# Kernel tuning notes

Hardware: AMD Instinct MI355X
Metric: run time of the kernel (lower is better)

The kernel has to match this reference:

```python
import jax, jax.numpy as jnp
import numpy as np

EPS = 1e-5        # torch BatchNorm2d default eps
G = 8             # DCNv4 groups
KP = 9            # 3x3 kernel points


def conv2d(x, w):
    return jax.lax.conv_general_dilated(
        x, w, window_strides=(1, 1), padding='SAME',
        dimension_numbers=('NCHW', 'OIHW', 'NCHW'))


def bn_eval(x, g_, b_, m_, v_):
    s = g_ / jnp.sqrt(v_ + EPS)
    return x * s[None, :, None, None] + (b_ - m_ * s)[None, :, None, None]


def silu(x):
    return x * jax.nn.sigmoid(x)


def dcnv4_core(value, offset, mask):
    # value: (N,H,W,G,Cg)  offset: (N,H,W,G,K,2) (x,y)  mask: (N,H,W,G,K) unnormalized (DCNv4: no softmax)
    N, H, W, Gn, Cg = value.shape
    r = jnp.arange(-1, 2, dtype=value.dtype)              # dilation=1, pad=1, 3x3 grid
    gy, gx = jnp.meshgrid(r, r, indexing='ij')
    grid_x = gx.ravel()  # (9,)
    grid_y = gy.ravel()
    px = jnp.arange(W, dtype=value.dtype)[None, None, :, None, None] + grid_x + offset[..., 0]
    py = jnp.arange(H, dtype=value.dtype)[None, :, None, None, None] + grid_y + offset[..., 1]
    x0 = jnp.floor(px); y0 = jnp.floor(py)
    lx = px - x0; ly = py - y0
    x0i = x0.astype(jnp.int32); y0i = y0.astype(jnp.int32)
    bidx = jnp.arange(N)[:, None, None, None, None]
    gidx = jnp.arange(Gn)[None, None, None, :, None]

    def tap(yi, xi, wgt):
        valid = (yi >= 0) & (yi < H) & (xi >= 0) & (xi < W)   # zero padding outside
        v = value[bidx, jnp.clip(yi, 0, H - 1), jnp.clip(xi, 0, W - 1), gidx]  # (N,H,W,G,K,Cg)
        return v * (wgt * valid)[..., None]

    s = (tap(y0i, x0i, (1 - ly) * (1 - lx))
         + tap(y0i, x0i + 1, (1 - ly) * lx)
         + tap(y0i + 1, x0i, ly * (1 - lx))
         + tap(y0i + 1, x0i + 1, ly * lx))
    return jnp.einsum('nhwgkc,nhwgk->nhwgc', s, mask)


def dcnv4(x, val_w, val_b, om_w, om_b, outp_w, outp_b):
    # x: NCHW. DCNv4 wrapper: flatten to tokens, value_proj, offset_mask linear on raw tokens,
    # deformable aggregation, output_proj, back to NCHW.
    N, C, H, W = x.shape
    t = x.transpose(0, 2, 3, 1).reshape(N, H * W, C)
    value = (t @ val_w.T + val_b).reshape(N, H, W, G, C // G)
    om = (t @ om_w.T + om_b).reshape(N, H, W, G, KP * 3)  # per group: 2K offsets then K masks
    offset = om[..., :2 * KP].reshape(N, H, W, G, KP, 2)
    mask = om[..., 2 * KP:]
    out = dcnv4_core(value, offset, mask).reshape(N, H * W, C)
    out = out @ outp_w.T + outp_b
    return out.reshape(N, H, W, C).transpose(0, 3, 1, 2)


def setup_inputs() -> dict:
    key = jax.random.key(0)
    ks = jax.random.split(key, 32)
    W_SC = 0.05
    d = {}
    d['x'] = jax.random.normal(ks[0], (4, 256, 64, 64), jnp.float32)
    d['cv1_w'] = jax.random.normal(ks[1], (128, 256, 3, 3), jnp.float32) * W_SC
    d['cv1_bn_g'] = jax.random.uniform(ks[2], (128,), jnp.float32, 0.5, 1.5)
    d['cv1_bn_b'] = jax.random.normal(ks[3], (128,), jnp.float32) * 0.1
    d['cv1_bn_m'] = jax.random.normal(ks[4], (128,), jnp.float32) * 0.1
    d['cv1_bn_v'] = jax.random.uniform(ks[5], (128,), jnp.float32, 0.5, 1.5)
    d['cv2_w'] = jax.random.normal(ks[6], (256, 128, 3, 3), jnp.float32) * W_SC
    d['cv2_bn_g'] = jax.random.uniform(ks[7], (256,), jnp.float32, 0.5, 1.5)
    d['cv2_bn_b'] = jax.random.normal(ks[8], (256,), jnp.float32) * 0.1
    d['cv2_bn_m'] = jax.random.normal(ks[9], (256,), jnp.float32) * 0.1
    d['cv2_bn_v'] = jax.random.uniform(ks[10], (256,), jnp.float32, 0.5, 1.5)
    d['val_w'] = jax.random.normal(ks[11], (256, 256), jnp.float32) * W_SC
    d['val_b'] = jax.random.normal(ks[12], (256,), jnp.float32) * 0.01
    d['om_w'] = jax.random.normal(ks[13], (216, 256), jnp.float32) * 0.02
    d['om_b'] = jax.random.normal(ks[14], (216,), jnp.float32) * 0.01
    d['outp_w'] = jax.random.normal(ks[15], (256, 256), jnp.float32) * W_SC
    d['outp_b'] = jax.random.normal(ks[16], (256,), jnp.float32) * 0.01
    d['bn3_g'] = jax.random.uniform(ks[17], (256,), jnp.float32, 0.5, 1.5)
    d['bn3_b'] = jax.random.normal(ks[18], (256,), jnp.float32) * 0.1
    d['bn3_m'] = jax.random.normal(ks[19], (256,), jnp.float32) * 0.1
    d['bn3_v'] = jax.random.uniform(ks[20], (256,), jnp.float32, 0.5, 1.5)
    d['pw1_w'] = jax.random.normal(ks[21], (768, 256, 1, 1), jnp.float32) * W_SC
    d['pw1_b'] = jax.random.normal(ks[22], (768,), jnp.float32) * 0.01
    d['pw2_w'] = jax.random.normal(ks[23], (256, 768, 1, 1), jnp.float32) * W_SC
    d['pw2_b'] = jax.random.normal(ks[24], (256,), jnp.float32) * 0.01
    return d


def reference(x, cv1_w, cv1_bn_g, cv1_bn_b, cv1_bn_m, cv1_bn_v,
              cv2_w, cv2_bn_g, cv2_bn_b, cv2_bn_m, cv2_bn_v,
              val_w, val_b, om_w, om_b, outp_w, outp_b,
              bn3_g, bn3_b, bn3_m, bn3_v, pw1_w, pw1_b, pw2_w, pw2_b):
    # cv2(cv1(x)) branch: Conv = Conv2d(no bias) + BN + SiLU
    y = silu(bn_eval(conv2d(x, cv1_w), cv1_bn_g, cv1_bn_b, cv1_bn_m, cv1_bn_v))
    y = silu(bn_eval(conv2d(y, cv2_w), cv2_bn_g, cv2_bn_b, cv2_bn_m, cv2_bn_v))
    # dcn branch: DCNv4 -> BN -> 1x1 conv (+SiLU) -> 1x1 conv
    d = dcnv4(x, val_w, val_b, om_w, om_b, outp_w, outp_b)
    d = bn_eval(d, bn3_g, bn3_b, bn3_m, bn3_v)
    d = silu(conv2d(d, pw1_w) + pw1_b[None, :, None, None])
    d = conv2d(d, pw2_w) + pw2_b[None, :, None, None]
    return x + y + d
```

## Files before the change

kernel.cpp:

```cpp
#include <hip/hip_runtime.h>
#include <math.h>

typedef __attribute__((ext_vector_type(8))) __bf16 bf16x8;
typedef __attribute__((ext_vector_type(8))) unsigned short us8;
typedef __attribute__((ext_vector_type(4))) unsigned short us4;
typedef __attribute__((ext_vector_type(4))) float f32x4;
typedef __attribute__((ext_vector_type(4))) int i32x4;
typedef unsigned int uint32;

#define EPSV 1e-5f

__device__ __forceinline__ float silu_f(float v) { return v / (1.f + __expf(-v)); }

__device__ __forceinline__ unsigned short f2bf(float f) {
  uint32 u = __builtin_bit_cast(uint32, f);
  u += 0x7fffu + ((u >> 16) & 1u);
  return (unsigned short)(u >> 16);
}
__device__ __forceinline__ float bf2f(unsigned short h) {
  uint32 u = ((uint32)h) << 16;
  return __builtin_bit_cast(float, u);
}

__device__ __forceinline__ int xswz(int b, int n) {
  return (b & 7) * (n >> 3) + (b >> 3);
}

__device__ __forceinline__ void gl_lds16(const void* g, void* l) {
  __builtin_amdgcn_global_load_lds(
      (const __attribute__((address_space(1))) unsigned int*)g,
      (__attribute__((address_space(3))) unsigned int*)l, 16, 0, 0);
}

template <int EPI, int CIN, int BN>
__device__ __forceinline__ void gemm_body(
    int rb, int cb, int k0, int KL,
    const unsigned short* __restrict__ A, const unsigned short* __restrict__ Bw,
    const float* __restrict__ bias, int K, int Co, void* __restrict__ outv,
    const float* __restrict__ e0, const float* __restrict__ e1,
    const float* __restrict__ e2, const float* __restrict__ e3,
    const unsigned short* __restrict__ zpage, bf16x8* smem) {
  constexpr int NFR = BN / 32;
  constexpr int NB = BN / 64;
  constexpr int CPB = 512 + BN * 4;
  const int t = threadIdx.x;
  const int lane = t & 63;
  const int wv = t >> 6;
  const int wr = wv >> 1, wc = wv & 1;

  f32x4 acc[4][NFR];
#pragma unroll
  for (int i = 0; i < 4; i++)
#pragma unroll
    for (int j = 0; j < NFR; j++) acc[i][j] = (f32x4){0.f, 0.f, 0.f, 0.f};

  const unsigned short* Abase[2];
  int aprow[2], apcol[2], akoff[2];
#pragma unroll
  for (int i = 0; i < 2; i++) {
    int c = t + 256 * i;
    int row = (c >> 6) * 16 + (c & 15);
    int koff = ((c >> 4) & 3) * 8;
    akoff[i] = koff;
    int grow = rb + row;
    if constexpr (CIN > 0) {
      int n = grow >> 12, p = grow & 4095;
      aprow[i] = p >> 6;
      apcol[i] = p & 63;
      Abase[i] = A + (size_t)n * 4096 * CIN;
    } else {
      Abase[i] = A + (size_t)grow * K + koff;
    }
  }
  const unsigned short* Bbase[NB];
#pragma unroll
  for (int i = 0; i < NB; i++) {
    int c = t + 256 * i;
    int col = cb + (c >> 6) * 16 + (c & 15);
    int koff = ((c >> 4) & 3) * 8;
    Bbase[i] = (col < Co) ? (Bw + (size_t)col * K + koff) : zpage;
  }
  auto addrA = [&](int i, int kb) -> const unsigned short* {
    if constexpr (CIN > 0) {
      int tap = kb / CIN;
      int ci = (kb & (CIN - 1)) + akoff[i];
      int dy = tap / 3 - 1, dx = tap % 3 - 1;
      int h = aprow[i] + dy, w = apcol[i] + dx;
      if (((unsigned)h < 64u) & ((unsigned)w < 64u))
        return &Abase[i][(size_t)(h * 64 + w) * CIN + ci];
      return zpage;
    } else {
      return Abase[i] + kb;
    }
  };
  auto stage = [&](int buf, int kb) {
    bf16x8* base = &smem[buf * CPB];
    gl_lds16(addrA(0, kb), (void*)&base[t]);
    gl_lds16(addrA(1, kb), (void*)&base[t + 256]);
    gl_lds16((Bbase[0] == zpage) ? zpage : Bbase[0] + kb, (void*)&base[512 + t]);
    if constexpr (NB == 2)
      gl_lds16((Bbase[1] == zpage) ? zpage : Bbase[1] + kb,
               (void*)&base[512 + t + 256]);
  };

  const int nt = KL >> 5;
  stage(0, k0);
  __syncthreads();
  int cur = 0;
  for (int it = 0; it < nt; ++it) {
    if (it + 1 < nt) stage(cur ^ 1, k0 + ((it + 1) << 5));
    const bf16x8* Ab = &smem[cur * CPB];
    const bf16x8* Bb = Ab + 512;
    bf16x8 af[4], bfr[NFR];
#pragma unroll
    for (int mi = 0; mi < 4; mi++) af[mi] = Ab[(wr * 4 + mi) * 64 + lane];
#pragma unroll
    for (int ni = 0; ni < NFR; ni++) bfr[ni] = Bb[(wc * NFR + ni) * 64 + lane];
    __builtin_amdgcn_s_setprio(1);
#pragma unroll
    for (int mi = 0; mi < 4; mi++)
#pragma unroll
      for (int ni = 0; ni < NFR; ni++)
        acc[mi][ni] = __builtin_amdgcn_mfma_f32_16x16x32_bf16(af[mi], bfr[ni],
                                                              acc[mi][ni], 0, 0, 0);
    __builtin_amdgcn_s_setprio(0);
    __syncthreads();
    cur ^= 1;
  }

  const int lr = lane & 15, kg4 = (lane >> 4) * 4;
#pragma unroll
  for (int mi = 0; mi < 4; mi++) {
#pragma unroll
    for (int ni = 0; ni < NFR; ni++) {
      int gcol = cb + wc * (BN / 2) + ni * 16 + lr;
      if (gcol >= Co) continue;
      float bval, s = 1.f, tt = 0.f;
      if (EPI == 2 || EPI == 7) bval = 0.f;
      else if (EPI == 5) bval = (gcol < 256) ? bias[gcol] : e0[gcol - 256];
      else bval = bias[gcol];
      if (EPI == 2 || EPI == 3) {
        s = e0[gcol] * rsqrtf(e3[gcol] + EPSV);
        tt = e1[gcol] - e2[gcol] * s;
      }
      if (EPI == 6) {
        int grow0 = rb + wr * 64 + mi * 16 + kg4;
        int n = grow0 >> 12, p0 = grow0 & 4095;
        size_t oix = ((size_t)(n * 256 + gcol)) * 4096 + p0;
        f32x4 xv = *(const f32x4*)&((const float*)e0)[oix];
        const unsigned short* y2p = (const unsigned short*)e1;
        f32x4 ov;
#pragma unroll
        for (int j = 0; j < 4; j++) {
          float y2 = bf2f(y2p[((size_t)(n * 4096 + p0 + j)) * 256 + gcol]);
          ov[j] = acc[mi][ni][j] + bval + xv[j] + y2;
        }
        *(f32x4*)&((float*)outv)[oix] = ov;
        continue;
      }
#pragma unroll
      for (int j = 0; j < 4; j++) {
        int grow = rb + wr * 64 + mi * 16 + kg4 + j;
        float v = acc[mi][ni][j] + bval;
        if (EPI == 2) v = silu_f(v * s + tt);
        if (EPI == 3) v = v * s + tt;
        if (EPI == 4) v = silu_f(v);
        if (EPI == 5) {
          if (gcol < 256)
            ((unsigned short*)outv)[(size_t)grow * 256 + gcol] = f2bf(v);
          else
            ((float*)e1)[(size_t)grow * 216 + (gcol - 256)] = v;
        } else {
          ((unsigned short*)outv)[(size_t)grow * Co + gcol] = f2bf(v);
        }
      }
    }
  }
}

__device__ __forceinline__ void dcn_body(
    int bid, const unsigned short* __restrict__ value,
    const float* __restrict__ om, unsigned short* __restrict__ out,
    void* smemraw) {
  f32x4* wgt = (f32x4*)smemraw;
  i32x4* adr = (i32x4*)((char*)smemraw + 288 * 16);
  const int n = bid >> 10;
  const int p0 = (bid & 1023) * 4;
  const int t = threadIdx.x;

  for (int idx = t; idx < 288; idx += 256) {
    int pi = idx / 72;
    int gk = idx - pi * 72;
    int g = gk / 9, k = gk - g * 9;
    int p = p0 + pi;
    int h0 = p >> 6, w0 = p & 63;
    const float* omp = om + ((size_t)(n * 4096 + p)) * 216 + g * 27;
    float ox = omp[2 * k], oy = omp[2 * k + 1], mk = omp[18 + k];
    float px = (float)(w0 + (k % 3) - 1) + ox;
    float py = (float)(h0 + (k / 3) - 1) + oy;
    float x0f = floorf(px), y0f = floorf(py);
    float lx = px - x0f, ly = py - y0f;
    int x0 = (int)x0f, y0 = (int)y0f;
    int x1 = x0 + 1, y1 = y0 + 1;
    bool vx0 = (unsigned)x0 < 64u, vx1 = (unsigned)x1 < 64u;
    bool vy0 = (unsigned)y0 < 64u, vy1 = (unsigned)y1 < 64u;
    int cx0 = min(max(x0, 0), 63), cx1 = min(max(x1, 0), 63);
    int cy0 = min(max(y0, 0), 63), cy1 = min(max(y1, 0), 63);
    f32x4 w4;
    w4[0] = (1.f - ly) * (1.f - lx) * mk * (float)(vy0 && vx0);
    w4[1] = (1.f - ly) * lx * mk * (float)(vy0 && vx1);
    w4[2] = ly * (1.f - lx) * mk * (float)(vy1 && vx0);
    w4[3] = ly * lx * mk * (float)(vy1 && vx1);
    i32x4 a4;
    a4[0] = (cy0 * 64 + cx0) * 256;
    a4[1] = (cy0 * 64 + cx1) * 256;
    a4[2] = (cy1 * 64 + cx0) * 256;
    a4[3] = (cy1 * 64 + cx1) * 256;
    wgt[idx] = w4;
    adr[idx] = a4;
  }
  __syncthreads();

  const int pi = t >> 6;
  const int g = (t >> 3) & 7;
  const int l = t & 7;
  const int p = p0 + pi;
  const unsigned short* vb = value + ((size_t)n * 4096) * 256 + g * 32 + l * 4;
  const int bix = (pi * 8 + g) * 9;
  float a0 = 0.f, a1 = 0.f, a2 = 0.f, a3 = 0.f;
#pragma unroll
  for (int k = 0; k < 9; k++) {
    f32x4 wv = wgt[bix + k];
    i32x4 av = adr[bix + k];
    us4 q0 = *(const us4*)(vb + av[0]);
    us4 q1 = *(const us4*)(vb + av[1]);
    us4 q2 = *(const us4*)(vb + av[2]);
    us4 q3 = *(const us4*)(vb + av[3]);
    a0 += wv[0] * bf2f(q0[0]) + wv[1] * bf2f(q1[0]) + wv[2] * bf2f(q2[0]) + wv[3] * bf2f(q3[0]);
    a1 += wv[0] * bf2f(q0[1]) + wv[1] * bf2f(q1[1]) + wv[2] * bf2f(q2[1]) + wv[3] * bf2f(q3[1]);
    a2 += wv[0] * bf2f(q0[2]) + wv[1] * bf2f(q1[2]) + wv[2] * bf2f(q2[2]) + wv[3] * bf2f(q3[2]);
    a3 += wv[0] * bf2f(q0[3]) + wv[1] * bf2f(q1[3]) + wv[2] * bf2f(q2[3]) + wv[3] * bf2f(q3[3]);
  }
  us4 o;
  o[0] = f2bf(a0); o[1] = f2bf(a1); o[2] = f2bf(a2); o[3] = f2bf(a3);
  *(us4*)&out[((size_t)(n * 4096 + p)) * 256 + g * 32 + l * 4] = o;
}

__global__ __launch_bounds__(256) void prep_k(
    const float* __restrict__ x, unsigned short* __restrict__ xt,
    const float* __restrict__ c1, unsigned short* __restrict__ o1,
    const float* __restrict__ c2, unsigned short* __restrict__ o2,
    const float* __restrict__ a0, unsigned short* __restrict__ b0,
    const float* __restrict__ a1, unsigned short* __restrict__ b1,
    const float* __restrict__ a2, unsigned short* __restrict__ b2,
    const float* __restrict__ a3, unsigned short* __restrict__ b3,
    const float* __restrict__ a4, unsigned short* __restrict__ b4,
    uint32* __restrict__ zp) {
  __shared__ float lds[64][65];
  int b = blockIdx.x;
  const int t = threadIdx.x;
  if (b == 0 && t < 32) zp[t] = 0u;
  if (b < 1024) {
    const int p0 = (b & 63) * 64, c0 = ((b >> 6) & 3) * 64, n = b >> 8;
    const int pp = t & 63, ccb = t >> 6;
    const float* xb = x + ((size_t)n * 256 + c0) * 4096 + p0;
#pragma unroll
    for (int i = 0; i < 16; i++) {
      int cc = ccb * 16 + i;
      lds[pp][cc] = xb[(size_t)cc * 4096 + pp];
    }
    __syncthreads();
#pragma unroll
    for (int i = 0; i < 2; i++) {
      int pp2 = (t >> 3) + i * 32;
      int c8 = (t & 7) * 8;
      us8 v;
#pragma unroll
      for (int j = 0; j < 8; j++) v[j] = f2bf(lds[pp2][c8 + j]);
      *(us8*)&xt[((size_t)(n * 4096 + p0 + pp2)) * 256 + c0 + c8] = v;
    }
    return;
  }
  if (b < 1152) {
    int idx = (b - 1024) * 256 + t;
    int co = idx >> 8, ci = idx & 255;
    const float* src = c1 + (size_t)(co * 256 + ci) * 9;
#pragma unroll
    for (int tap = 0; tap < 9; tap++)
      o1[(size_t)(co * 9 + tap) * 256 + ci] = f2bf(src[tap]);
    return;
  }
  if (b < 1280) {
    int idx = (b - 1152) * 256 + t;
    int co = idx >> 7, ci = idx & 127;
    const float* src = c2 + (size_t)(co * 128 + ci) * 9;
#pragma unroll
    for (int tap = 0; tap < 9; tap++)
      o2[(size_t)(co * 9 + tap) * 128 + ci] = f2bf(src[tap]);
    return;
  }
  int idx = (b - 1280) * 256 + t;
  const float* s;
  unsigned short* d;
  int off;
  if (idx < 65536)       { s = a0; d = b0; off = idx; }
  else if (idx < 120832) { s = a1; d = b1; off = idx - 65536; }
  else if (idx < 186368) { s = a2; d = b2; off = idx - 120832; }
  else if (idx < 382976) { s = a3; d = b3; off = idx - 186368; }
  else if (idx < 579584) { s = a4; d = b4; off = idx - 382976; }
  else return;
  d[off] = f2bf(s[off]);
}

__global__ __launch_bounds__(256) void fused_s1(
    const unsigned short* __restrict__ xt,
    const unsigned short* __restrict__ wc1, unsigned short* __restrict__ part,
    const unsigned short* __restrict__ wval, const float* __restrict__ val_b,
    const float* __restrict__ om_b, float* __restrict__ omf,
    unsigned short* __restrict__ valt, const unsigned short* __restrict__ zpage) {
  __shared__ bf16x8 smem[2048];
  int l = xswz(blockIdx.x, 1024);
  if ((l & 1) == 0) {
    int c = l >> 1;
    int s = c >> 7, mt = c & 127;
    gemm_body<7, 256, 128>(mt * 128, 0, s * 576, 576, xt, wc1, nullptr, 2304,
                           128, part + (size_t)s * 2097152, nullptr, nullptr,
                           nullptr, nullptr, zpage, smem);
  } else {
    int v = l >> 1;
    gemm_body<5, 0, 128>((v >> 2) * 128, (v & 3) * 128, 0, 256, xt, wval, val_b,
                         256, 472, valt, om_b, (const float*)omf, nullptr,
                         nullptr, zpage, smem);
  }
}

__global__ __launch_bounds__(256) void fused_r(
    const unsigned short* __restrict__ part, const float* __restrict__ g1,
    const float* __restrict__ bb1, const float* __restrict__ m1,
    const float* __restrict__ v1, unsigned short* __restrict__ y1t,
    const unsigned short* __restrict__ valt, const float* __restrict__ omf,
    unsigned short* __restrict__ dcnt) {
  __shared__ char rsm[9216];
  int l = xswz(blockIdx.x, 5120);
  int q = l / 5, r5 = l - q * 5;
  if (r5 == 0) {
    int g = q * 256 + threadIdx.x;
    int grow = g >> 4;
    int co8 = (g & 15) << 3;
    size_t base = (size_t)grow * 128 + co8;
    float sum[8] = {0.f, 0.f, 0.f, 0.f, 0.f, 0.f, 0.f, 0.f};
#pragma unroll
    for (int s = 0; s < 4; s++) {
      us8 pv = *(const us8*)&part[base + (size_t)s * 2097152];
#pragma unroll
      for (int j = 0; j < 8; j++) sum[j] += bf2f(pv[j]);
    }
    us8 o;
#pragma unroll
    for (int j = 0; j < 8; j++) {
      int co = co8 + j;
      float sc = g1[co] * rsqrtf(v1[co] + EPSV);
      float tt = bb1[co] - m1[co] * sc;
      o[j] = f2bf(silu_f(sum[j] * sc + tt));
    }
    *(us8*)&y1t[base] = o;
  } else {
    dcn_body(q * 4 + r5 - 1, valt, omf, dcnt, (void*)rsm);
  }
}

__global__ __launch_bounds__(256) void fused_s2(
    const unsigned short* __restrict__ y1t,
    const unsigned short* __restrict__ wc2, const float* __restrict__ g2,
    const float* __restrict__ bb2, const float* __restrict__ m2,
    const float* __restrict__ v2, unsigned short* __restrict__ y2t,
    const unsigned short* __restrict__ dcnt, const unsigned short* __restrict__ woutp,
    const float* __restrict__ outp_b, const float* __restrict__ g3,
    const float* __restrict__ bb3, const float* __restrict__ m3,
    const float* __restrict__ v3, unsigned short* __restrict__ d1t,
    const unsigned short* __restrict__ zpage) {
  __shared__ bf16x8 smem[1536];
  int l = xswz(blockIdx.x, 1024);
  if ((l & 1) == 0) {
    int c = l >> 1;
    gemm_body<2, 128, 64>((c >> 2) * 128, (c & 3) * 64, 0, 1152, y1t, wc2,
                          nullptr, 1152, 256, y2t, g2, bb2, m2, v2, zpage, smem);
  } else {
    int v = l >> 1;
    gemm_body<3, 0, 64>((v >> 2) * 128, (v & 3) * 64, 0, 256, dcnt, woutp,
                        outp_b, 256, 256, d1t, g3, bb3, m3, v3, zpage, smem);
  }
}

template <int EPI, int CIN, int BN, int NCB, int GRID>
__global__ __launch_bounds__(256) void gemm_k(
    const unsigned short* __restrict__ A, const unsigned short* __restrict__ Bw,
    const float* __restrict__ bias, int K, int Co, void* __restrict__ outv,
    const float* __restrict__ e0, const float* __restrict__ e1,
    const float* __restrict__ e2, const float* __restrict__ e3,
    const unsigned short* __restrict__ zpage) {
  __shared__ bf16x8 smem[2 * (512 + BN * 4)];
  int l = xswz(blockIdx.x, GRID);
  gemm_body<EPI, CIN, BN>((l / NCB) * 128, (l % NCB) * BN, 0, K, A, Bw, bias,
                          K, Co, outv, e0, e1, e2, e3, zpage, smem);
}

extern "C" void kernel_launch(void* const* d_in, const int* in_sizes, int n_in,
                              void* d_out, int out_size, void* d_ws,
                              size_t ws_size, hipStream_t stream) {
  const float* x      = (const float*)d_in[0];
  const float* cv1_w  = (const float*)d_in[1];
  const float* cv1_g  = (const float*)d_in[2];
  const float* cv1_b  = (const float*)d_in[3];
  const float* cv1_m  = (const float*)d_in[4];
  const float* cv1_v  = (const float*)d_in[5];
  const float* cv2_w  = (const float*)d_in[6];
  const float* cv2_g  = (const float*)d_in[7];
  const float* cv2_b  = (const float*)d_in[8];
  const float* cv2_m  = (const float*)d_in[9];
  const float* cv2_v  = (const float*)d_in[10];
  const float* val_w  = (const float*)d_in[11];
  const float* val_b  = (const float*)d_in[12];
  const float* om_w   = (const float*)d_in[13];
  const float* om_b   = (const float*)d_in[14];
  const float* outp_w = (const float*)d_in[15];
  const float* outp_b = (const float*)d_in[16];
  const float* bn3_g  = (const float*)d_in[17];
  const float* bn3_b  = (const float*)d_in[18];
  const float* bn3_m  = (const float*)d_in[19];
  const float* bn3_v  = (const float*)d_in[20];
  const float* pw1_w  = (const float*)d_in[21];
  const float* pw1_b  = (const float*)d_in[22];
  const float* pw2_w  = (const float*)d_in[23];
  const float* pw2_b  = (const float*)d_in[24];
  float* out = (float*)d_out;

  char* w = (char*)d_ws;
  auto alloc = [&](size_t bytes) {
    char* p = w;
    w += (bytes + 255) & ~(size_t)255;
    return p;
  };
  unsigned short* xt    = (unsigned short*)alloc(16384ull * 256 * 2);
  unsigned short* y1t   = (unsigned short*)alloc(16384ull * 128 * 2);
  unsigned short* y2t   = (unsigned short*)alloc(16384ull * 256 * 2);
  unsigned short* valt  = (unsigned short*)alloc(16384ull * 256 * 2);
  float*          omf   = (float*)alloc(16384ull * 216 * 4);
  unsigned short* dcnt  = (unsigned short*)alloc(16384ull * 256 * 2);
  unsigned short* d1t   = (unsigned short*)alloc(16384ull * 256 * 2);
  unsigned short* p1t   = (unsigned short*)alloc(16384ull * 768 * 2);
  unsigned short* part = d1t;
  unsigned short* wc1   = (unsigned short*)alloc(128ull * 2304 * 2);
  unsigned short* wc2   = (unsigned short*)alloc(256ull * 1152 * 2);
  unsigned short* wval  = (unsigned short*)alloc(256ull * 256 * 2);
  unsigned short* wom   = (unsigned short*)alloc(216ull * 256 * 2);
  unsigned short* woutp = (unsigned short*)alloc(256ull * 256 * 2);
  unsigned short* wpw1  = (unsigned short*)alloc(768ull * 256 * 2);
  unsigned short* wpw2  = (unsigned short*)alloc(256ull * 768 * 2);
  unsigned short* zpage = (unsigned short*)alloc(256);

  prep_k<<<3544, 256, 0, stream>>>(x, xt, cv1_w, wc1, cv2_w, wc2, val_w, wval,
                                   om_w, wom, outp_w, woutp, pw1_w, wpw1,
                                   pw2_w, wpw2, (uint32*)zpage);

  fused_s1<<<1024, 256, 0, stream>>>(xt, wc1, part, wval, val_b, om_b, omf,
                                     valt, zpage);

  fused_r<<<5120, 256, 0, stream>>>(part, cv1_g, cv1_b, cv1_m, cv1_v, y1t,
                                    valt, omf, dcnt);

  fused_s2<<<1024, 256, 0, stream>>>(y1t, wc2, cv2_g, cv2_b, cv2_m, cv2_v, y2t,
                                     dcnt, woutp, outp_b, bn3_g, bn3_b, bn3_m,
                                     bn3_v, d1t, zpage);

  gemm_k<4, 0, 128, 6, 768><<<768, 256, 0, stream>>>(
      d1t, wpw1, pw1_b, 256, 768, p1t, nullptr, nullptr, nullptr, nullptr, zpage);
  gemm_k<6, 0, 64, 4, 512><<<512, 256, 0, stream>>>(
      p1t, wpw2, pw2_b, 768, 256, out, x, (const float*)y2t, nullptr, nullptr, zpage);
}
```

Baseline: 176.6 us.

## Split cv2 conv K-dimension into two partials and fuse reduction with pw1 GEMM

The cv2 3x3 conv GEMM now runs split-K in two halves that write bf16 partial sums, which doubles its block count. The BN+SiLU reduction of those partials moves into a new kernel that shares a launch with the pw1 GEMM. The XCD-aware block swizzle is removed from every kernel and replaced with linear or 2D block indexing. This adds partial-buffer traffic, an extra bf16 rounding of the partials, and possibly worse L2 locality without the swizzle.

```diff
diff --git a/kernel.cpp b/kernel.cpp
--- a/kernel.cpp
+++ b/kernel.cpp
@@ -20,10 +20,6 @@
 __device__ __forceinline__ float bf2f(unsigned short h) {
   uint32 u = ((uint32)h) << 16;
   return __builtin_bit_cast(float, u);
-}
-
-__device__ __forceinline__ int xswz(int b, int n) {
-  return (b & 7) * (n >> 3) + (b >> 3);
 }
 
 __device__ __forceinline__ void gl_lds16(const void* g, void* l) {
@@ -319,16 +315,15 @@
     const float* __restrict__ om_b, float* __restrict__ omf,
     unsigned short* __restrict__ valt, const unsigned short* __restrict__ zpage) {
   __shared__ bf16x8 smem[2048];
-  int l = xswz(blockIdx.x, 1024);
-  if ((l & 1) == 0) {
-    int c = l >> 1;
-    int s = c >> 7, mt = c & 127;
+  int b = blockIdx.x;
+  if (b < 512) {
+    int s = b >> 7, mt = b & 127;
     gemm_body<7, 256, 128>(mt * 128, 0, s * 576, 576, xt, wc1, nullptr, 2304,
                            128, part + (size_t)s * 2097152, nullptr, nullptr,
                            nullptr, nullptr, zpage, smem);
   } else {
-    int v = l >> 1;
-    gemm_body<5, 0, 128>((v >> 2) * 128, (v & 3) * 128, 0, 256, xt, wval, val_b,
+    b -= 512;
+    gemm_body<5, 0, 128>((b >> 2) * 128, (b & 3) * 128, 0, 256, xt, wval, val_b,
                          256, 472, valt, om_b, (const float*)omf, nullptr,
                          nullptr, zpage, smem);
   }
@@ -341,10 +336,9 @@
     const unsigned short* __restrict__ valt, const float* __restrict__ omf,
     unsigned short* __restrict__ dcnt) {
   __shared__ char rsm[9216];
-  int l = xswz(blockIdx.x, 5120);
-  int q = l / 5, r5 = l - q * 5;
-  if (r5 == 0) {
-    int g = q * 256 + threadIdx.x;
+  int b = blockIdx.x;
+  if (b < 1024) {
+    int g = b * 256 + threadIdx.x;
     int grow = g >> 4;
     int co8 = (g & 15) << 3;
     size_t base = (size_t)grow * 128 + co8;
@@ -365,34 +359,68 @@
     }
     *(us8*)&y1t[base] = o;
   } else {
-    dcn_body(q * 4 + r5 - 1, valt, omf, dcnt, (void*)rsm);
+    dcn_body(b - 1024, valt, omf, dcnt, (void*)rsm);
   }
 }
 
 __global__ __launch_bounds__(256) void fused_s2(
     const unsigned short* __restrict__ y1t,
-    const unsigned short* __restrict__ wc2, const float* __restrict__ g2,
-    const float* __restrict__ bb2, const float* __restrict__ m2,
-    const float* __restrict__ v2, unsigned short* __restrict__ y2t,
+    const unsigned short* __restrict__ wc2, unsigned short* __restrict__ part2,
     const unsigned short* __restrict__ dcnt, const unsigned short* __restrict__ woutp,
     const float* __restrict__ outp_b, const float* __restrict__ g3,
     const float* __restrict__ bb3, const float* __restrict__ m3,
     const float* __restrict__ v3, unsigned short* __restrict__ d1t,
     const unsigned short* __restrict__ zpage) {
   __shared__ bf16x8 smem[1536];
-  int l = xswz(blockIdx.x, 1024);
-  if ((l & 1) == 0) {
-    int c = l >> 1;
-    gemm_body<2, 128, 64>((c >> 2) * 128, (c & 3) * 64, 0, 1152, y1t, wc2,
-                          nullptr, 1152, 256, y2t, g2, bb2, m2, v2, zpage, smem);
+  int b = blockIdx.x;
+  if (b < 1024) {
+    int s = b >> 9, c = b & 511;
+    gemm_body<7, 128, 64>((c >> 2) * 128, (c & 3) * 64, s * 576, 576, y1t, wc2,
+                          nullptr, 1152, 256, part2 + (size_t)s * 4194304,
+                          nullptr, nullptr, nullptr, nullptr, zpage, smem);
   } else {
-    int v = l >> 1;
-    gemm_body<3, 0, 64>((v >> 2) * 128, (v & 3) * 64, 0, 256, dcnt, woutp,
+    b -= 1024;
+    gemm_body<3, 0, 64>((b >> 2) * 128, (b & 3) * 64, 0, 256, dcnt, woutp,
                         outp_b, 256, 256, d1t, g3, bb3, m3, v3, zpage, smem);
   }
 }
 
-template <int EPI, int CIN, int BN, int NCB, int GRID>
+__global__ __launch_bounds__(256) void pw1_mix(
+    const unsigned short* __restrict__ d1t, const unsigned short* __restrict__ wpw1,
+    const float* __restrict__ pw1_b, unsigned short* __restrict__ p1t,
+    const unsigned short* __restrict__ part2, const float* __restrict__ g2,
+    const float* __restrict__ bb2, const float* __restrict__ m2,
+    const float* __restrict__ v2, unsigned short* __restrict__ y2t,
+    const unsigned short* __restrict__ zpage) {
+  __shared__ bf16x8 smem[2048];
+  int b = blockIdx.x;
+  if (b < 768) {
+    gemm_body<4, 0, 128>((b / 6) * 128, (b % 6) * 128, 0, 256, d1t, wpw1,
+                         pw1_b, 256, 768, p1t, nullptr, nullptr, nullptr,
+                         nullptr, zpage, smem);
+  } else {
+    int g = (b - 768) * 256 + threadIdx.x;
+    size_t base = (size_t)g * 32;
+#pragma unroll
+    for (int q = 0; q < 4; q++) {
+      size_t off = base + q * 8;
+      us8 p0 = *(const us8*)&part2[off];
+      us8 p1 = *(const us8*)&part2[off + 4194304];
+      int co8 = (int)(off & 255);
+      us8 o;
+#pragma unroll
+      for (int j = 0; j < 8; j++) {
+        int co = co8 + j;
+        float sc = g2[co] * rsqrtf(v2[co] + EPSV);
+        float tt = bb2[co] - m2[co] * sc;
+        o[j] = f2bf(silu_f((bf2f(p0[j]) + bf2f(p1[j])) * sc + tt));
+      }
+      *(us8*)&y2t[off] = o;
+    }
+  }
+}
+
+template <int EPI, int CIN, int BN>
 __global__ __launch_bounds__(256) void gemm_k(
     const unsigned short* __restrict__ A, const unsigned short* __restrict__ Bw,
     const float* __restrict__ bias, int K, int Co, void* __restrict__ outv,
@@ -400,8 +428,7 @@
     const float* __restrict__ e2, const float* __restrict__ e3,
     const unsigned short* __restrict__ zpage) {
   __shared__ bf16x8 smem[2 * (512 + BN * 4)];
-  int l = xswz(blockIdx.x, GRID);
-  gemm_body<EPI, CIN, BN>((l / NCB) * 128, (l % NCB) * BN, 0, K, A, Bw, bias,
+  gemm_body<EPI, CIN, BN>(blockIdx.y * 128, blockIdx.x * BN, 0, K, A, Bw, bias,
                           K, Co, outv, e0, e1, e2, e3, zpage, smem);
 }
 
@@ -450,6 +477,7 @@
   unsigned short* d1t   = (unsigned short*)alloc(16384ull * 256 * 2);
   unsigned short* p1t   = (unsigned short*)alloc(16384ull * 768 * 2);
   unsigned short* part = d1t;
+  unsigned short* part2 = (unsigned short*)alloc(2ull * 4194304 * 2);
   unsigned short* wc1   = (unsigned short*)alloc(128ull * 2304 * 2);
   unsigned short* wc2   = (unsigned short*)alloc(256ull * 1152 * 2);
   unsigned short* wval  = (unsigned short*)alloc(256ull * 256 * 2);
@@ -469,12 +497,12 @@
   fused_r<<<5120, 256, 0, stream>>>(part, cv1_g, cv1_b, cv1_m, cv1_v, y1t,
                                     valt, omf, dcnt);
 
-  fused_s2<<<1024, 256, 0, stream>>>(y1t, wc2, cv2_g, cv2_b, cv2_m, cv2_v, y2t,
-                                     dcnt, woutp, outp_b, bn3_g, bn3_b, bn3_m,
-                                     bn3_v, d1t, zpage);
-
-  gemm_k<4, 0, 128, 6, 768><<<768, 256, 0, stream>>>(
-      d1t, wpw1, pw1_b, 256, 768, p1t, nullptr, nullptr, nullptr, nullptr, zpage);
-  gemm_k<6, 0, 64, 4, 512><<<512, 256, 0, stream>>>(
+  fused_s2<<<1536, 256, 0, stream>>>(y1t, wc2, part2, dcnt, woutp, outp_b,
+                                     bn3_g, bn3_b, bn3_m, bn3_v, d1t, zpage);
+
+  pw1_mix<<<1280, 256, 0, stream>>>(d1t, wpw1, pw1_b, p1t, part2, cv2_g, cv2_b,
+                                    cv2_m, cv2_v, y2t, zpage);
+
+  gemm_k<6, 0, 64><<<dim3(4, 128), 256, 0, stream>>>(
       p1t, wpw2, pw2_b, 768, 256, out, x, (const float*)y2t, nullptr, nullptr, zpage);
 }
```

New measurement: 174.1 us. No clear change (-1.4%).

## Widen DCN gather to 8 channels per thread and drop XCD block swizzle

Applied to the files above, without the earlier changes.

The deformable sampling body now handles 8 pixels per block, and each thread gathers 16-byte vectors covering 8 channels instead of 8-byte vectors covering 4. This halves the number of DCN blocks and doubles the per-block shared-memory tables for weights and addresses. Separately, the XCD-aware block-index swizzle is removed from all fused and GEMM kernels, which now use plain linear or 2D grid mapping. This trades L2 locality across chiplets for simpler indexing and may change how the branches interleave on the device.

```diff
diff --git a/kernel.cpp b/kernel.cpp
--- a/kernel.cpp
+++ b/kernel.cpp
@@ -20,10 +20,6 @@
 __device__ __forceinline__ float bf2f(unsigned short h) {
   uint32 u = ((uint32)h) << 16;
   return __builtin_bit_cast(float, u);
-}
-
-__device__ __forceinline__ int xswz(int b, int n) {
-  return (b & 7) * (n >> 3) + (b >> 3);
 }
 
 __device__ __forceinline__ void gl_lds16(const void* g, void* l) {
@@ -183,12 +179,12 @@
     const float* __restrict__ om, unsigned short* __restrict__ out,
     void* smemraw) {
   f32x4* wgt = (f32x4*)smemraw;
-  i32x4* adr = (i32x4*)((char*)smemraw + 288 * 16);
-  const int n = bid >> 10;
-  const int p0 = (bid & 1023) * 4;
+  i32x4* adr = (i32x4*)((char*)smemraw + 576 * 16);
+  const int n = bid >> 9;
+  const int p0 = (bid & 511) * 8;
   const int t = threadIdx.x;
 
-  for (int idx = t; idx < 288; idx += 256) {
+  for (int idx = t; idx < 576; idx += 256) {
     int pi = idx / 72;
     int gk = idx - pi * 72;
     int g = gk / 9, k = gk - g * 9;
@@ -221,29 +217,30 @@
   }
   __syncthreads();
 
-  const int pi = t >> 6;
-  const int g = (t >> 3) & 7;
-  const int l = t & 7;
+  const int pi = t >> 5;
+  const int g = (t >> 2) & 7;
+  const int l = t & 3;
   const int p = p0 + pi;
-  const unsigned short* vb = value + ((size_t)n * 4096) * 256 + g * 32 + l * 4;
+  const unsigned short* vb = value + ((size_t)n * 4096) * 256 + g * 32 + l * 8;
   const int bix = (pi * 8 + g) * 9;
-  float a0 = 0.f, a1 = 0.f, a2 = 0.f, a3 = 0.f;
+  float a[8] = {0.f, 0.f, 0.f, 0.f, 0.f, 0.f, 0.f, 0.f};
 #pragma unroll
   for (int k = 0; k < 9; k++) {
     f32x4 wv = wgt[bix + k];
     i32x4 av = adr[bix + k];
-    us4 q0 = *(const us4*)(vb + av[0]);
-    us4 q1 = *(const us4*)(vb + av[1]);
-    us4 q2 = *(const us4*)(vb + av[2]);
-    us4 q3 = *(const us4*)(vb + av[3]);
-    a0 += wv[0] * bf2f(q0[0]) + wv[1] * bf2f(q1[0]) + wv[2] * bf2f(q2[0]) + wv[3] * bf2f(q3[0]);
-    a1 += wv[0] * bf2f(q0[1]) + wv[1] * bf2f(q1[1]) + wv[2] * bf2f(q2[1]) + wv[3] * bf2f(q3[1]);
-    a2 += wv[0] * bf2f(q0[2]) + wv[1] * bf2f(q1[2]) + wv[2] * bf2f(q2[2]) + wv[3] * bf2f(q3[2]);
-    a3 += wv[0] * bf2f(q0[3]) + wv[1] * bf2f(q1[3]) + wv[2] * bf2f(q2[3]) + wv[3] * bf2f(q3[3]);
-  }
-  us4 o;
-  o[0] = f2bf(a0); o[1] = f2bf(a1); o[2] = f2bf(a2); o[3] = f2bf(a3);
-  *(us4*)&out[((size_t)(n * 4096 + p)) * 256 + g * 32 + l * 4] = o;
+    us8 q0 = *(const us8*)(vb + av[0]);
+    us8 q1 = *(const us8*)(vb + av[1]);
+    us8 q2 = *(const us8*)(vb + av[2]);
+    us8 q3 = *(const us8*)(vb + av[3]);
+#pragma unroll
+    for (int j = 0; j < 8; j++)
+      a[j] += wv[0] * bf2f(q0[j]) + wv[1] * bf2f(q1[j]) +
+              wv[2] * bf2f(q2[j]) + wv[3] * bf2f(q3[j]);
+  }
+  us8 o;
+#pragma unroll
+  for (int j = 0; j < 8; j++) o[j] = f2bf(a[j]);
+  *(us8*)&out[((size_t)(n * 4096 + p)) * 256 + g * 32 + l * 8] = o;
 }
 
 __global__ __launch_bounds__(256) void prep_k(
@@ -319,16 +316,15 @@
     const float* __restrict__ om_b, float* __restrict__ omf,
     unsigned short* __restrict__ valt, const unsigned short* __restrict__ zpage) {
   __shared__ bf16x8 smem[2048];
-  int l = xswz(blockIdx.x, 1024);
-  if ((l & 1) == 0) {
-    int c = l >> 1;
-    int s = c >> 7, mt = c & 127;
+  int b = blockIdx.x;
+  if (b < 512) {
+    int s = b >> 7, mt = b & 127;
     gemm_body<7, 256, 128>(mt * 128, 0, s * 576, 576, xt, wc1, nullptr, 2304,
                            128, part + (size_t)s * 2097152, nullptr, nullptr,
                            nullptr, nullptr, zpage, smem);
   } else {
-    int v = l >> 1;
-    gemm_body<5, 0, 128>((v >> 2) * 128, (v & 3) * 128, 0, 256, xt, wval, val_b,
+    b -= 512;
+    gemm_body<5, 0, 128>((b >> 2) * 128, (b & 3) * 128, 0, 256, xt, wval, val_b,
                          256, 472, valt, om_b, (const float*)omf, nullptr,
                          nullptr, zpage, smem);
   }
@@ -340,11 +336,10 @@
     const float* __restrict__ v1, unsigned short* __restrict__ y1t,
     const unsigned short* __restrict__ valt, const float* __restrict__ omf,
     unsigned short* __restrict__ dcnt) {
-  __shared__ char rsm[9216];
-  int l = xswz(blockIdx.x, 5120);
-  int q = l / 5, r5 = l - q * 5;
-  if (r5 == 0) {
-    int g = q * 256 + threadIdx.x;
+  __shared__ char rsm[18432];
+  int b = blockIdx.x;
+  if (b < 1024) {
+    int g = b * 256 + threadIdx.x;
     int grow = g >> 4;
     int co8 = (g & 15) << 3;
     size_t base = (size_t)grow * 128 + co8;
@@ -365,7 +360,7 @@
     }
     *(us8*)&y1t[base] = o;
   } else {
-    dcn_body(q * 4 + r5 - 1, valt, omf, dcnt, (void*)rsm);
+    dcn_body(b - 1024, valt, omf, dcnt, (void*)rsm);
   }
 }
 
@@ -380,19 +375,18 @@
     const float* __restrict__ v3, unsigned short* __restrict__ d1t,
     const unsigned short* __restrict__ zpage) {
   __shared__ bf16x8 smem[1536];
-  int l = xswz(blockIdx.x, 1024);
-  if ((l & 1) == 0) {
-    int c = l >> 1;
-    gemm_body<2, 128, 64>((c >> 2) * 128, (c & 3) * 64, 0, 1152, y1t, wc2,
+  int b = blockIdx.x;
+  if (b < 512) {
+    gemm_body<2, 128, 64>((b >> 2) * 128, (b & 3) * 64, 0, 1152, y1t, wc2,
                           nullptr, 1152, 256, y2t, g2, bb2, m2, v2, zpage, smem);
   } else {
-    int v = l >> 1;
-    gemm_body<3, 0, 64>((v >> 2) * 128, (v & 3) * 64, 0, 256, dcnt, woutp,
+    b -= 512;
+    gemm_body<3, 0, 64>((b >> 2) * 128, (b & 3) * 64, 0, 256, dcnt, woutp,
                         outp_b, 256, 256, d1t, g3, bb3, m3, v3, zpage, smem);
   }
 }
 
-template <int EPI, int CIN, int BN, int NCB, int GRID>
+template <int EPI, int CIN, int BN>
 __global__ __launch_bounds__(256) void gemm_k(
     const unsigned short* __restrict__ A, const unsigned short* __restrict__ Bw,
     const float* __restrict__ bias, int K, int Co, void* __restrict__ outv,
@@ -400,8 +394,7 @@
     const float* __restrict__ e2, const float* __restrict__ e3,
     const unsigned short* __restrict__ zpage) {
   __shared__ bf16x8 smem[2 * (512 + BN * 4)];
-  int l = xswz(blockIdx.x, GRID);
-  gemm_body<EPI, CIN, BN>((l / NCB) * 128, (l % NCB) * BN, 0, K, A, Bw, bias,
+  gemm_body<EPI, CIN, BN>(blockIdx.y * 128, blockIdx.x * BN, 0, K, A, Bw, bias,
                           K, Co, outv, e0, e1, e2, e3, zpage, smem);
 }
 
@@ -466,15 +459,15 @@
   fused_s1<<<1024, 256, 0, stream>>>(xt, wc1, part, wval, val_b, om_b, omf,
                                      valt, zpage);
 
-  fused_r<<<5120, 256, 0, stream>>>(part, cv1_g, cv1_b, cv1_m, cv1_v, y1t,
+  fused_r<<<3072, 256, 0, stream>>>(part, cv1_g, cv1_b, cv1_m, cv1_v, y1t,
                                     valt, omf, dcnt);
 
   fused_s2<<<1024, 256, 0, stream>>>(y1t, wc2, cv2_g, cv2_b, cv2_m, cv2_v, y2t,
                                      dcnt, woutp, outp_b, bn3_g, bn3_b, bn3_m,
                                      bn3_v, d1t, zpage);
 
-  gemm_k<4, 0, 128, 6, 768><<<768, 256, 0, stream>>>(
+  gemm_k<4, 0, 128><<<dim3(6, 128), 256, 0, stream>>>(
       d1t, wpw1, pw1_b, 256, 768, p1t, nullptr, nullptr, nullptr, nullptr, zpage);
-  gemm_k<6, 0, 64, 4, 512><<<512, 256, 0, stream>>>(
+  gemm_k<6, 0, 64><<<dim3(4, 128), 256, 0, stream>>>(
       p1t, wpw2, pw2_b, 768, 256, out, x, (const float*)y2t, nullptr, nullptr, zpage);
 }
```

Result: faster. 158.8 us (-10.1%).
